# Optimization experiments

Hardware: AMD Instinct MI355X
Metric: run time of the kernel (lower is better)

## Reference

```python
import jax, jax.numpy as jnp
import numpy as np
from jax import lax

B, T, V, E, H, L = 128, 256, 50000, 300, 512, 96


def masked_lstm(x, mask, W, U, b):
    """Keras-semantics masked LSTM, return_sequences=True.
    x: [B,T,D], mask: [B,T] bool. Gate order i,f,c,o (Keras).
    Masked steps carry h,c forward (output at masked step = previous output)."""
    Hs = U.shape[0]
    # input-to-hidden done as one big GEMM outside the scan
    xg = jnp.einsum('btd,dg->btg', x, W) + b  # [B,T,4H]
    h0 = jnp.zeros((x.shape[0], Hs), x.dtype)
    c0 = jnp.zeros((x.shape[0], Hs), x.dtype)

    def step(carry, inp):
        h, c = carry
        g_x, m = inp  # [B,4H], [B]
        g = g_x + h @ U
        i = jax.nn.sigmoid(g[:, :Hs])
        f = jax.nn.sigmoid(g[:, Hs:2 * Hs])
        cand = jnp.tanh(g[:, 2 * Hs:3 * Hs])
        o = jax.nn.sigmoid(g[:, 3 * Hs:])
        c_new = f * c + i * cand
        h_new = o * jnp.tanh(c_new)
        m = m[:, None]
        h_new = jnp.where(m, h_new, h)
        c_new = jnp.where(m, c_new, c)
        return (h_new, c_new), h_new

    (_, _), hs = lax.scan(step, (h0, c0), (xg.transpose(1, 0, 2), mask.T))
    return hs.transpose(1, 0, 2)  # [B,T,H]


def setup_inputs() -> dict:
    key = jax.random.key(0)
    ks = jax.random.split(key, 11)
    word_ids = jax.random.randint(ks[0], (B, T), 0, V, dtype=jnp.int32)
    predicate_ids = jax.random.randint(ks[1], (B, T), 0, 2, dtype=jnp.int32)
    emb = jax.random.normal(ks[2], (V, E), jnp.float32) * 0.1
    W1 = jax.random.normal(ks[3], (E + 1, 4 * H), jnp.float32) * 0.05
    U1 = jax.random.normal(ks[4], (H, 4 * H), jnp.float32) * 0.05
    b1 = jnp.zeros((4 * H,), jnp.float32)
    W2 = jax.random.normal(ks[5], (H, 4 * H), jnp.float32) * 0.05
    U2 = jax.random.normal(ks[6], (H, 4 * H), jnp.float32) * 0.05
    b2 = jnp.zeros((4 * H,), jnp.float32)
    Wd = jax.random.normal(ks[7], (H, L), jnp.float32) * 0.05
    bd = jnp.zeros((L,), jnp.float32)
    return {"word_ids": word_ids, "predicate_ids": predicate_ids,
            "emb": emb, "W1": W1, "U1": U1, "b1": b1,
            "W2": W2, "U2": U2, "b2": b2, "Wd": Wd, "bd": bd,
            "training": 0}


def reference(word_ids, predicate_ids, emb, W1, U1, b1, W2, U2, b2, Wd, bd, training):
    # training=0 -> dropout disabled (keep_prob=1.0 anyway)
    mask = word_ids != 0  # mask_zero semantics of the Embedding layer
    x = emb[word_ids]  # [B,T,E]
    flag = predicate_ids.astype(x.dtype)[..., None]  # [B,T,1]
    x = jnp.concatenate([x, flag], axis=2)  # [B,T,E+1]
    h1 = masked_lstm(x, mask, W1, U1, b1)
    h2 = masked_lstm(h1, mask, W2, U2, b2)
    enc = h2.reshape(-1, U1.shape[0])  # [B*T, H]
    return jax.nn.softmax(enc @ Wd + bd, axis=-1)  # [B*T, L]
```

## Files before the change

### kernel.cpp

```cpp
#include <hip/hip_runtime.h>
#include <hip/hip_bf16.h>

#define T_SEQ 256
#define HID 512
#define G4 2048
#define ASTR 80

typedef __attribute__((ext_vector_type(8))) short short8;
typedef __attribute__((ext_vector_type(4))) float floatx4;
typedef __attribute__((ext_vector_type(4))) int intx4;

__device__ inline unsigned short f2bf(float f) {
  union { __hip_bfloat16 h; unsigned short u; } cv;
  cv.h = __float2bfloat16(f);
  return cv.u;
}
__device__ inline float bf2f(unsigned short u) {
  union { unsigned short u; __hip_bfloat16 h; } cv;
  cv.u = u;
  return __bfloat162float(cv.h);
}
__device__ inline float fsigmoid(float x) {
  return __builtin_amdgcn_rcpf(1.0f + __expf(-x));
}
__device__ inline float ftanh(float x) {
  float e = __expf(2.0f * x);
  return 1.0f - 2.0f * __builtin_amdgcn_rcpf(e + 1.0f);
}

__device__ __forceinline__ void bar_lgkm() {
  asm volatile("s_waitcnt lgkmcnt(0)\n\ts_barrier" ::: "memory");
}

__global__ __launch_bounds__(256) void transpose_bf16(const float* __restrict__ src,
                                                      unsigned short* __restrict__ dst,
                                                      int K, int N, int Kpad) {
  __shared__ float tile[32][33];
  int n0 = blockIdx.x * 32, k0 = blockIdx.y * 32;
  int tx = threadIdx.x & 31, ty = threadIdx.x >> 5;
#pragma unroll
  for (int i = 0; i < 32; i += 8) {
    int k = k0 + ty + i, n = n0 + tx;
    tile[ty + i][tx] = (k < K) ? src[(size_t)k * N + n] : 0.0f;
  }
  __syncthreads();
#pragma unroll
  for (int i = 0; i < 32; i += 8) {
    int n = n0 + ty + i, k = k0 + tx;
    dst[(size_t)n * Kpad + k] = f2bf(tile[tx][ty + i]);
  }
}

__global__ __launch_bounds__(256) void gemm_xg1(const float* __restrict__ emb,
                                                const int* __restrict__ wid,
                                                const int* __restrict__ pred,
                                                const unsigned short* __restrict__ Bt,
                                                unsigned short* __restrict__ C) {
  int m0 = blockIdx.x * 64;
  int tid = threadIdx.x, lane = tid & 63, w = tid >> 6;
  __shared__ __align__(16) short As[64][328];
  __shared__ __align__(16) short Bs[2][64][40];
  {
    int grow = tid >> 2, gpart = tid & 3;
    int wrow = wid[m0 + grow];
    float pflag = (float)pred[m0 + grow];
    const float* erow = emb + (size_t)wrow * 300;
#pragma unroll
    for (int i = 0; i < 10; i++) {
      int c0 = gpart * 80 + i * 8;
      float f[8];
      if (c0 + 8 <= 300) {
        float4 x0 = *(const float4*)(erow + c0);
        float4 x1 = *(const float4*)(erow + c0 + 4);
        f[0] = x0.x; f[1] = x0.y; f[2] = x0.z; f[3] = x0.w;
        f[4] = x1.x; f[5] = x1.y; f[6] = x1.z; f[7] = x1.w;
      } else {
#pragma unroll
        for (int j = 0; j < 8; j++) {
          int k = c0 + j;
          f[j] = (k < 300) ? erow[k] : ((k == 300) ? pflag : 0.0f);
        }
      }
      short8 v;
#pragma unroll
      for (int j = 0; j < 8; j++) v[j] = (short)f2bf(f[j]);
      *(short8*)&As[grow][c0] = v;
    }
  }
  int brow = tid >> 2, bpart = tid & 3;
  for (int n0 = 0; n0 < 2048; n0 += 64) {
    *(short8*)&Bs[0][brow][bpart * 8] =
        *(const short8*)(Bt + (size_t)(n0 + brow) * 320 + bpart * 8);
    bar_lgkm();
    floatx4 acc[4];
#pragma unroll
    for (int i = 0; i < 4; i++) acc[i] = (floatx4){0.f, 0.f, 0.f, 0.f};
#pragma unroll
    for (int ks = 0; ks < 10; ks++) {
      if (ks < 9)
        *(short8*)&Bs[(ks + 1) & 1][brow][bpart * 8] =
            *(const short8*)(Bt + (size_t)(n0 + brow) * 320 + (ks + 1) * 32 + bpart * 8);
      short8 afr = *(const short8*)&As[w * 16 + (lane & 15)][ks * 32 + (lane >> 4) * 8];
#pragma unroll
      for (int nc = 0; nc < 4; nc++) {
        short8 bfr = *(const short8*)&Bs[ks & 1][nc * 16 + (lane & 15)][(lane >> 4) * 8];
        acc[nc] = __builtin_amdgcn_mfma_f32_16x16x32_bf16(afr, bfr, acc[nc], 0, 0, 0);
      }
      bar_lgkm();
    }
#pragma unroll
    for (int nc = 0; nc < 4; nc++)
#pragma unroll
      for (int r = 0; r < 4; r++) {
        int rr = m0 + w * 16 + ((lane >> 4) << 2) + r;
        int cc = n0 + nc * 16 + (lane & 15);
        C[(size_t)rr * G4 + cc] = f2bf(acc[nc][r]);
      }
  }
}

__device__ __forceinline__ void stg_issue(const unsigned int* rowbase, int c16,
                                          intx4 (&v)[8], unsigned done) {
#pragma unroll
  for (int i = 0; i < 8; i++) {
    if (!(done & (1u << i))) {
      const unsigned int* p = rowbase + 8 * c16 + 128 * (i >> 1) + 4 * (i & 1);
      asm volatile("global_load_dwordx4 %0, %1, off sc0 sc1" : "=v"(v[i]) : "v"(p) : "memory");
    }
  }
}
__device__ __forceinline__ void stg_check(unsigned want, char* AhRow, int sw, int c16,
                                          intx4 (&v)[8], unsigned& done) {
  asm volatile("s_waitcnt vmcnt(0)" ::: "memory");
#pragma unroll
  for (int i = 0; i < 8; i++) {
    if (!(done & (1u << i))) {
      intx4 a = v[i];
      unsigned u0 = (unsigned)a.x, u1 = (unsigned)a.y, u2 = (unsigned)a.z, u3 = (unsigned)a.w;
      bool ok = ((u0 >> 16) == want) & ((u1 >> 16) == want) & ((u2 >> 16) == want) &
                ((u3 >> 16) == want);
      if (ok) {
        uint2 pp;
        pp.x = (u0 & 0xffffu) | (u1 << 16);
        pp.y = (u2 & 0xffffu) | (u3 << 16);
        int s = c16 + 16 * (i >> 1);
        *(uint2*)(AhRow + ((s * 16) ^ sw) + (i & 1) * 8) = pp;
        done |= (1u << i);
      }
    }
  }
}
__device__ __forceinline__ void stg_finish(const unsigned int* rowbase, unsigned want,
                                           char* AhRow, int sw, int c16,
                                           intx4 (&v)[8], unsigned& done) {
  stg_check(want, AhRow, sw, c16, v, done);
  while (done != 0xFFu) {
    __builtin_amdgcn_s_sleep(1);
    stg_issue(rowbase, c16, v, done);
    stg_check(want, AhRow, sw, c16, v, done);
  }
}

__global__ __launch_bounds__(256, 1) __attribute__((amdgpu_waves_per_eu(1, 1)))
void lstm_merged(
    const unsigned short* __restrict__ xg1,
    const unsigned short* __restrict__ Ut1, const float* __restrict__ b1,
    const unsigned short* __restrict__ Wt2, const unsigned short* __restrict__ Ut2,
    const float* __restrict__ b2, const int* __restrict__ wid,
    unsigned int* ex, unsigned short* h2seq) {
  const int blk = blockIdx.x;
  const int bgrp = blk & 7, jblk = blk >> 3;
  const int b0 = bgrp * 16, j0 = jblk * 16;
  const int tid = threadIdx.x, lane = tid & 63, w = tid >> 6;

  __shared__ __align__(16) char AhA[16 * 1024];
  __shared__ __align__(16) char AhB[16 * 1024];
  __shared__ __align__(16) char U2L[64 * 1024];
  __shared__ float gds[4][16][16];
  __shared__ float cst1[16][16];
  __shared__ float cst2[16][16];

  const int row = tid >> 4, c16 = tid & 15;
  const int sw = (row & 7) << 4;
  char* AhRowA = AhA + row * 1024;
  char* AhRowB = AhB + row * 1024;
  const int ucol = w * 512 + j0 + (lane & 15);
  const int* widp = wid + (size_t)(b0 + row) * T_SEQ;

  short8 uf1[16], wf2[16];
  {
    const unsigned short* p1 = Ut1 + (size_t)ucol * 512 + ((lane >> 4) * 8);
    const unsigned short* p2 = Wt2 + (size_t)ucol * 512 + ((lane >> 4) * 8);
#pragma unroll
    for (int kk = 0; kk < 16; kk++) {
      uf1[kk] = *(const short8*)(p1 + kk * 32);
      wf2[kk] = *(const short8*)(p2 + kk * 32);
    }
  }
  for (int i = tid; i < 4096; i += 256) {
    int r = i >> 6, seg = i & 63;
    short8 v = *(const short8*)(Ut2 + (size_t)((r >> 4) * 512 + j0 + (r & 15)) * 512 + seg * 8);
    *(short8*)(U2L + r * 1024 + ((seg * 16) ^ ((r & 7) << 4))) = v;
  }
  float b1v[4], b2v[4];
#pragma unroll
  for (int g = 0; g < 4; g++) {
    b1v[g] = b1[g * 512 + j0 + c16];
    b2v[g] = b2[g * 512 + j0 + c16];
  }
  cst1[row][c16] = 0.0f;
  cst2[row][c16] = 0.0f;
  {
    short8 z = {0, 0, 0, 0, 0, 0, 0, 0};
    for (int i = tid; i < 1024; i += 256) {
      *(short8*)(AhA + i * 16) = z;
      *(short8*)(AhB + i * 16) = z;
    }
  }
  __syncthreads();

  const unsigned short* xgrow = xg1 + (size_t)(b0 + row) * T_SEQ * G4 + j0 + c16;
  unsigned short xc[4], xn[4];
#pragma unroll
  for (int g = 0; g < 4; g++) { xc[g] = xgrow[g * 512]; xn[g] = 0; }
  int mcur = widp[0];
  int mprev = 0;

  const size_t SLOT = (size_t)2 * 128 * 512;
  const int frow = lane & 15, kbase = (lane >> 4) * 16, fsw = (frow & 7) << 4;
  const int urow = w * 16 + (lane & 15);
  const int usw = (urow & 7) << 4;

  intx4 pendA[8], pendB[8];
  unsigned doneA = 0xFFu;

  for (int t = 0; t <= T_SEQ; t++) {
    if (t > 0) {
      const unsigned int* bA = ex + (size_t)((t - 1) & 1) * SLOT + (size_t)(b0 + row) * 512;
      stg_finish(bA, (unsigned)t, AhRowA, sw, c16, pendA, doneA);
    }
    bar_lgkm();

    floatx4 a1x = (floatx4){0.f, 0.f, 0.f, 0.f};
    floatx4 a1y = (floatx4){0.f, 0.f, 0.f, 0.f};
#pragma unroll
    for (int kk = 0; kk < 16; kk += 2) {
      short8 a0 = *(const short8*)(AhA + frow * 1024 + ((kk * 64 + kbase) ^ fsw));
      short8 a1f = *(const short8*)(AhA + frow * 1024 + (((kk + 1) * 64 + kbase) ^ fsw));
      a1x = __builtin_amdgcn_mfma_f32_16x16x32_bf16(a0, uf1[kk], a1x, 0, 0, 0);
      a1y = __builtin_amdgcn_mfma_f32_16x16x32_bf16(a1f, uf1[kk + 1], a1y, 0, 0, 0);
    }
    if (t < T_SEQ) {
#pragma unroll
      for (int r = 0; r < 4; r++)
        gds[w][((lane >> 4) << 2) + r][lane & 15] = a1x[r] + a1y[r];
    }
    bar_lgkm();

    if (t < T_SEQ) {
      float gi = gds[0][row][c16] + b1v[0] + bf2f(xc[0]);
      float gf = gds[1][row][c16] + b1v[1] + bf2f(xc[1]);
      float gc = gds[2][row][c16] + b1v[2] + bf2f(xc[2]);
      float go = gds[3][row][c16] + b1v[3] + bf2f(xc[3]);
      float iv = fsigmoid(gi), fv = fsigmoid(gf), cd = ftanh(gc), ov = fsigmoid(go);
      float cold = cst1[row][c16];
      float cn = fv * cold + iv * cd;
      float hn = ov * ftanh(cn);
      if (mcur == 0) {
        cn = cold;
        hn = bf2f(*(const unsigned short*)(AhRowA + (((j0 + c16) * 2) ^ sw)));
      }
      cst1[row][c16] = cn;
      unsigned v1 = (((unsigned)(t + 1)) << 16) | f2bf(hn);
      unsigned int* d1 = ex + (size_t)(t & 1) * SLOT + (size_t)(b0 + row) * 512 + j0 + c16;
      asm volatile("global_store_dword %0, %1, off sc0 sc1" ::"v"(d1), "v"(v1) : "memory");
    }
    if (t == 0) {
      unsigned v2 = 1u << 16;
      unsigned int* d2 = ex + (size_t)128 * 512 + (size_t)(b0 + row) * 512 + j0 + c16;
      asm volatile("global_store_dword %0, %1, off sc0 sc1" ::"v"(d2), "v"(v2) : "memory");
    }
    if (t + 1 < T_SEQ) {
      const unsigned short* xr = xgrow + (size_t)(t + 1) * G4;
#pragma unroll
      for (int g = 0; g < 4; g++) xn[g] = xr[g * 512];
    }

    if (t > 0) {
      unsigned doneB = 0;
      const unsigned int* bB = ex + (size_t)((t - 1) & 1) * SLOT + (size_t)128 * 512 +
                               (size_t)(b0 + row) * 512;
      stg_issue(bB, c16, pendB, doneB);

      floatx4 a2x = (floatx4){0.f, 0.f, 0.f, 0.f};
      floatx4 a2y = (floatx4){0.f, 0.f, 0.f, 0.f};
#pragma unroll
      for (int kk = 0; kk < 16; kk += 2) {
        short8 a0 = *(const short8*)(AhA + frow * 1024 + ((kk * 64 + kbase) ^ fsw));
        short8 a1f = *(const short8*)(AhA + frow * 1024 + (((kk + 1) * 64 + kbase) ^ fsw));
        a2x = __builtin_amdgcn_mfma_f32_16x16x32_bf16(a0, wf2[kk], a2x, 0, 0, 0);
        a2y = __builtin_amdgcn_mfma_f32_16x16x32_bf16(a1f, wf2[kk + 1], a2y, 0, 0, 0);
      }

      stg_finish(bB, (unsigned)t, AhRowB, sw, c16, pendB, doneB);
      bar_lgkm();

#pragma unroll
      for (int kk = 0; kk < 16; kk += 2) {
        short8 a0 = *(const short8*)(AhB + frow * 1024 + ((kk * 64 + kbase) ^ fsw));
        short8 u0 = *(const short8*)(U2L + urow * 1024 + ((kk * 64 + kbase) ^ usw));
        short8 a1f = *(const short8*)(AhB + frow * 1024 + (((kk + 1) * 64 + kbase) ^ fsw));
        short8 u1 = *(const short8*)(U2L + urow * 1024 + (((kk + 1) * 64 + kbase) ^ usw));
        a2x = __builtin_amdgcn_mfma_f32_16x16x32_bf16(a0, u0, a2x, 0, 0, 0);
        a2y = __builtin_amdgcn_mfma_f32_16x16x32_bf16(a1f, u1, a2y, 0, 0, 0);
      }
#pragma unroll
      for (int r = 0; r < 4; r++)
        gds[w][((lane >> 4) << 2) + r][lane & 15] = a2x[r] + a2y[r];
      bar_lgkm();

      {
        float gi = gds[0][row][c16] + b2v[0];
        float gf = gds[1][row][c16] + b2v[1];
        float gc = gds[2][row][c16] + b2v[2];
        float go = gds[3][row][c16] + b2v[3];
        float iv = fsigmoid(gi), fv = fsigmoid(gf), cd = ftanh(gc), ov = fsigmoid(go);
        float cold = cst2[row][c16];
        float cn = fv * cold + iv * cd;
        float hn = ov * ftanh(cn);
        if (mprev == 0) {
          cn = cold;
          hn = bf2f(*(const unsigned short*)(AhRowB + (((j0 + c16) * 2) ^ sw)));
        }
        cst2[row][c16] = cn;
        unsigned short hb = f2bf(hn);
        if (t < T_SEQ) {
          unsigned v2 = (((unsigned)(t + 1)) << 16) | hb;
          unsigned int* d2 = ex + (size_t)(t & 1) * SLOT + (size_t)128 * 512 +
                             (size_t)(b0 + row) * 512 + j0 + c16;
          asm volatile("global_store_dword %0, %1, off sc0 sc1" ::"v"(d2), "v"(v2) : "memory");
        }
        h2seq[((size_t)(b0 + row) * T_SEQ + (t - 1)) * HID + j0 + c16] = hb;
      }
      bar_lgkm();
    } else {
      bar_lgkm();
    }

    if (t < T_SEQ) {
      const unsigned int* bA2 = ex + (size_t)(t & 1) * SLOT + (size_t)(b0 + row) * 512;
      doneA = 0;
      stg_issue(bA2, c16, pendA, doneA);
    }
    mprev = mcur;
    mcur = (t + 1 < T_SEQ) ? widp[t + 1] : 0;
#pragma unroll
    for (int g = 0; g < 4; g++) xc[g] = xn[g];
  }
}

__global__ __launch_bounds__(256) void dense_softmax(const unsigned short* __restrict__ h2,
                                                     const unsigned short* __restrict__ Wdt,
                                                     const float* __restrict__ bd,
                                                     float* __restrict__ out) {
  int m0 = blockIdx.x * 64;
  int tid = threadIdx.x, lane = tid & 63, w = tid >> 6;
  __shared__ __align__(16) char As[64 * ASTR];
  __shared__ __align__(16) char Bs[96 * ASTR];
  floatx4 acc[6];
#pragma unroll
  for (int i = 0; i < 6; i++) acc[i] = (floatx4){0.f, 0.f, 0.f, 0.f};
  for (int k0 = 0; k0 < 512; k0 += 32) {
    {
      int row = tid >> 2, part = tid & 3;
      short8 v = *(const short8*)(h2 + (size_t)(m0 + row) * 512 + k0 + part * 8);
      *(short8*)(As + row * ASTR + part * 16) = v;
    }
    for (int u = tid; u < 96 * 4; u += 256) {
      int col = u >> 2, part = u & 3;
      short8 v = *(const short8*)(Wdt + (size_t)col * 512 + k0 + part * 8);
      *(short8*)(Bs + col * ASTR + part * 16) = v;
    }
    __syncthreads();
    int arow = w * 16 + (lane & 15);
    short8 a = *(const short8*)(As + arow * ASTR + (lane >> 4) * 16);
#pragma unroll
    for (int nc = 0; nc < 6; nc++) {
      int bcol = nc * 16 + (lane & 15);
      short8 b = *(const short8*)(Bs + bcol * ASTR + (lane >> 4) * 16);
      acc[nc] = __builtin_amdgcn_mfma_f32_16x16x32_bf16(a, b, acc[nc], 0, 0, 0);
    }
    __syncthreads();
  }
  float bv[6];
#pragma unroll
  for (int nc = 0; nc < 6; nc++) bv[nc] = bd[nc * 16 + (lane & 15)];
#pragma unroll
  for (int r = 0; r < 4; r++) {
    float v[6];
    float mx = -1e30f;
#pragma unroll
    for (int nc = 0; nc < 6; nc++) {
      v[nc] = acc[nc][r] + bv[nc];
      mx = fmaxf(mx, v[nc]);
    }
#pragma unroll
    for (int d = 1; d < 16; d <<= 1) mx = fmaxf(mx, __shfl_xor(mx, d));
    float s = 0.f;
#pragma unroll
    for (int nc = 0; nc < 6; nc++) {
      v[nc] = __expf(v[nc] - mx);
      s += v[nc];
    }
#pragma unroll
    for (int d = 1; d < 16; d <<= 1) s += __shfl_xor(s, d);
    float inv = 1.0f / s;
    int rr = m0 + w * 16 + ((lane >> 4) << 2) + r;
#pragma unroll
    for (int nc = 0; nc < 6; nc++) out[(size_t)rr * 96 + nc * 16 + (lane & 15)] = v[nc] * inv;
  }
}

extern "C" void kernel_launch(void* const* d_in, const int* in_sizes, int n_in,
                              void* d_out, int out_size, void* d_ws, size_t ws_size,
                              hipStream_t stream) {
  (void)in_sizes; (void)n_in; (void)out_size; (void)ws_size;
  const int* word_ids = (const int*)d_in[0];
  const int* pred = (const int*)d_in[1];
  const float* emb = (const float*)d_in[2];
  const float* W1 = (const float*)d_in[3];
  const float* U1 = (const float*)d_in[4];
  const float* b1 = (const float*)d_in[5];
  const float* W2 = (const float*)d_in[6];
  const float* U2 = (const float*)d_in[7];
  const float* b2 = (const float*)d_in[8];
  const float* Wd = (const float*)d_in[9];
  const float* bd = (const float*)d_in[10];
  float* out = (float*)d_out;

  const size_t EXBYTES = (size_t)2 * 2 * 128 * 512 * 4;

  char* p = (char*)d_ws;
  unsigned short* xg = (unsigned short*)p;   p += (size_t)32768 * 2048 * 2;
  unsigned short* h2s = (unsigned short*)p;  p += (size_t)32768 * 512 * 2;
  unsigned int* ex = (unsigned int*)p;       p += EXBYTES;
  unsigned short* Ut1 = (unsigned short*)p;  p += (size_t)2048 * 512 * 2;
  unsigned short* Ut2 = (unsigned short*)p;  p += (size_t)2048 * 512 * 2;
  unsigned short* Wt1 = (unsigned short*)p;  p += (size_t)2048 * 320 * 2;
  unsigned short* Wt2 = (unsigned short*)p;  p += (size_t)2048 * 512 * 2;
  unsigned short* Wdt = (unsigned short*)p;  p += (size_t)96 * 512 * 2;

  hipMemsetAsync(ex, 0, EXBYTES, stream);

  hipLaunchKernelGGL(transpose_bf16, dim3(64, 16), dim3(256), 0, stream, U1, Ut1, 512, 2048, 512);
  hipLaunchKernelGGL(transpose_bf16, dim3(64, 16), dim3(256), 0, stream, U2, Ut2, 512, 2048, 512);
  hipLaunchKernelGGL(transpose_bf16, dim3(64, 10), dim3(256), 0, stream, W1, Wt1, 301, 2048, 320);
  hipLaunchKernelGGL(transpose_bf16, dim3(64, 16), dim3(256), 0, stream, W2, Wt2, 512, 2048, 512);
  hipLaunchKernelGGL(transpose_bf16, dim3(3, 16), dim3(256), 0, stream, Wd, Wdt, 512, 96, 512);

  hipLaunchKernelGGL(gemm_xg1, dim3(512), dim3(256), 0, stream,
                     emb, word_ids, pred, Wt1, xg);
  hipLaunchKernelGGL(lstm_merged, dim3(256), dim3(256), 0, stream,
                     xg, Ut1, b1, Wt2, Ut2, b2, word_ids, ex, h2s);
  hipLaunchKernelGGL(dense_softmax, dim3(512), dim3(256), 0, stream, h2s, Wdt, bd, out);
}
```

Before: 1.430 ms.

## Replace layer-1 tagged-word exchange with per-step counter flags and bulk loads

Layer-1 hidden-state exchange between blocks no longer packs a step tag next to each bf16 value and polls every word. Each block now writes plain bf16 values into a per-timestep buffer. After a barrier it atomically bumps a per-batch-group counter, and consumers spin on that single counter before issuing four wide vector loads. The intent is to halve exchange traffic and replace per-element tag polling with one flag poll. The cost is an extra block-wide barrier with a full vmcnt drain, an atomic per step, and a strictly serial wait-then-load latency instead of the overlapped issue/check scheme.

After: 1.383 ms. 1.03x faster.

```diff
diff --git a/kernel.cpp b/kernel.cpp
--- a/kernel.cpp
+++ b/kernel.cpp
@@ -167,7 +167,8 @@
     const unsigned short* __restrict__ Ut1, const float* __restrict__ b1,
     const unsigned short* __restrict__ Wt2, const unsigned short* __restrict__ Ut2,
     const float* __restrict__ b2, const int* __restrict__ wid,
-    unsigned int* ex, unsigned short* h2seq) {
+    unsigned int* ex, unsigned int* flags1, unsigned short* h1bc,
+    unsigned short* h2seq) {
   const int blk = blockIdx.x;
   const int bgrp = blk & 7, jblk = blk >> 3;
   const int b0 = bgrp * 16, j0 = jblk * 16;
@@ -231,13 +232,20 @@
   const int urow = w * 16 + (lane & 15);
   const int usw = (urow & 7) << 4;
 
-  intx4 pendA[8], pendB[8];
-  unsigned doneA = 0xFFu;
+  intx4 pendB[8];
+  intx4 dA[4];
 
   for (int t = 0; t <= T_SEQ; t++) {
     if (t > 0) {
-      const unsigned int* bA = ex + (size_t)((t - 1) & 1) * SLOT + (size_t)(b0 + row) * 512;
-      stg_finish(bA, (unsigned)t, AhRowA, sw, c16, pendA, doneA);
+      asm volatile("s_waitcnt vmcnt(0)" ::: "memory");
+#pragma unroll
+      for (int i = 0; i < 4; i++)
+        *(intx4*)(AhRowA + (((c16 * 4 + i) * 16) ^ sw)) = dA[i];
+    }
+    if (t + 1 < T_SEQ) {
+      const unsigned short* xr = xgrow + (size_t)(t + 1) * G4;
+#pragma unroll
+      for (int g = 0; g < 4; g++) xn[g] = xr[g * 512];
     }
     bar_lgkm();
 
@@ -271,19 +279,14 @@
         hn = bf2f(*(const unsigned short*)(AhRowA + (((j0 + c16) * 2) ^ sw)));
       }
       cst1[row][c16] = cn;
-      unsigned v1 = (((unsigned)(t + 1)) << 16) | f2bf(hn);
-      unsigned int* d1 = ex + (size_t)(t & 1) * SLOT + (size_t)(b0 + row) * 512 + j0 + c16;
-      asm volatile("global_store_dword %0, %1, off sc0 sc1" ::"v"(d1), "v"(v1) : "memory");
+      unsigned hv = (unsigned)f2bf(hn);
+      const unsigned short* d1 = h1bc + ((size_t)t * 128 + b0 + row) * 512 + j0 + c16;
+      asm volatile("global_store_short %0, %1, off sc0 sc1" ::"v"(d1), "v"(hv) : "memory");
     }
     if (t == 0) {
       unsigned v2 = 1u << 16;
       unsigned int* d2 = ex + (size_t)128 * 512 + (size_t)(b0 + row) * 512 + j0 + c16;
       asm volatile("global_store_dword %0, %1, off sc0 sc1" ::"v"(d2), "v"(v2) : "memory");
-    }
-    if (t + 1 < T_SEQ) {
-      const unsigned short* xr = xgrow + (size_t)(t + 1) * G4;
-#pragma unroll
-      for (int g = 0; g < 4; g++) xn[g] = xr[g * 512];
     }
 
     if (t > 0) {
@@ -317,7 +320,13 @@
 #pragma unroll
       for (int r = 0; r < 4; r++)
         gds[w][((lane >> 4) << 2) + r][lane & 15] = a2x[r] + a2y[r];
-      bar_lgkm();
+
+      asm volatile("s_waitcnt vmcnt(0) lgkmcnt(0)\n\ts_barrier" ::: "memory");
+      if (tid == 0 && t < T_SEQ) {
+        unsigned one = 1;
+        unsigned int* fp = flags1 + (size_t)t * 8 + bgrp;
+        asm volatile("global_atomic_add %0, %1, off sc1" ::"v"(fp), "v"(one) : "memory");
+      }
 
       {
         float gi = gds[0][row][c16] + b2v[0];
@@ -342,15 +351,32 @@
         }
         h2seq[((size_t)(b0 + row) * T_SEQ + (t - 1)) * HID + j0 + c16] = hb;
       }
-      bar_lgkm();
     } else {
-      bar_lgkm();
+      asm volatile("s_waitcnt vmcnt(0) lgkmcnt(0)\n\ts_barrier" ::: "memory");
+      if (tid == 0) {
+        unsigned one = 1;
+        unsigned int* fp = flags1 + bgrp;
+        asm volatile("global_atomic_add %0, %1, off sc1" ::"v"(fp), "v"(one) : "memory");
+      }
     }
 
     if (t < T_SEQ) {
-      const unsigned int* bA2 = ex + (size_t)(t & 1) * SLOT + (size_t)(b0 + row) * 512;
-      doneA = 0;
-      stg_issue(bA2, c16, pendA, doneA);
+      const unsigned int* fp = flags1 + (size_t)t * 8 + bgrp;
+      while (true) {
+        unsigned v;
+        asm volatile("global_load_dword %0, %1, off sc0 sc1\n\ts_waitcnt vmcnt(0)"
+                     : "=v"(v) : "v"(fp) : "memory");
+        if (v >= 32u) break;
+        __builtin_amdgcn_s_sleep(1);
+      }
+      const unsigned short* pA = h1bc + ((size_t)t * 128 + b0 + row) * 512 + c16 * 32;
+      asm volatile(
+          "global_load_dwordx4 %0, %4, off\n\t"
+          "global_load_dwordx4 %1, %4, off offset:16\n\t"
+          "global_load_dwordx4 %2, %4, off offset:32\n\t"
+          "global_load_dwordx4 %3, %4, off offset:48"
+          : "=v"(dA[0]), "=v"(dA[1]), "=v"(dA[2]), "=v"(dA[3])
+          : "v"(pA) : "memory");
     }
     mprev = mcur;
     mcur = (t + 1 < T_SEQ) ? widp[t + 1] : 0;
@@ -439,18 +465,21 @@
   float* out = (float*)d_out;
 
   const size_t EXBYTES = (size_t)2 * 2 * 128 * 512 * 4;
+  const size_t FLAGBYTES = (size_t)T_SEQ * 8 * 4;
 
   char* p = (char*)d_ws;
   unsigned short* xg = (unsigned short*)p;   p += (size_t)32768 * 2048 * 2;
   unsigned short* h2s = (unsigned short*)p;  p += (size_t)32768 * 512 * 2;
   unsigned int* ex = (unsigned int*)p;       p += EXBYTES;
+  unsigned int* flags1 = (unsigned int*)p;   p += FLAGBYTES;
+  unsigned short* h1bc = (unsigned short*)p; p += (size_t)T_SEQ * 128 * 512 * 2;
   unsigned short* Ut1 = (unsigned short*)p;  p += (size_t)2048 * 512 * 2;
   unsigned short* Ut2 = (unsigned short*)p;  p += (size_t)2048 * 512 * 2;
   unsigned short* Wt1 = (unsigned short*)p;  p += (size_t)2048 * 320 * 2;
   unsigned short* Wt2 = (unsigned short*)p;  p += (size_t)2048 * 512 * 2;
   unsigned short* Wdt = (unsigned short*)p;  p += (size_t)96 * 512 * 2;
 
-  hipMemsetAsync(ex, 0, EXBYTES, stream);
+  hipMemsetAsync(ex, 0, EXBYTES + FLAGBYTES, stream);
 
   hipLaunchKernelGGL(transpose_bf16, dim3(64, 16), dim3(256), 0, stream, U1, Ut1, 512, 2048, 512);
   hipLaunchKernelGGL(transpose_bf16, dim3(64, 16), dim3(256), 0, stream, U2, Ut2, 512, 2048, 512);
@@ -461,6 +490,6 @@
   hipLaunchKernelGGL(gemm_xg1, dim3(512), dim3(256), 0, stream,
                      emb, word_ids, pred, Wt1, xg);
   hipLaunchKernelGGL(lstm_merged, dim3(256), dim3(256), 0, stream,
-                     xg, Ut1, b1, Wt2, Ut2, b2, word_ids, ex, h2s);
+                     xg, Ut1, b1, Wt2, Ut2, b2, word_ids, ex, flags1, h1bc, h2s);
   hipLaunchKernelGGL(dense_softmax, dim3(512), dim3(256), 0, stream, h2s, Wdt, bd, out);
 }
```
